# Optimization experiments

Hardware: AMD Instinct MI355X
Metric: run time of the kernel (lower is better)

The kernel has to match this reference:

```python
import jax, jax.numpy as jnp
import numpy as np

B = 4          # graphs
N = 8192       # coarse nodes (2048/graph)
M = 65536      # fine (skip) nodes (16384/graph)
E = 131072     # edges (32768/graph)
T = 16         # global tokens per graph
F_IN = 16      # dim of x and x_skip (concat -> in_channels = 32)
HID, OUT = 32, 16
ED, GD, EMB, H = 3, 1024, 64, 4
K = 3


def _make_pe(t, d):
    # PositionalEncoding buffer (sin/cos), deterministic constant
    position = np.arange(t, dtype=np.float32)[:, None]
    div = np.exp(np.arange(0, d, 2, dtype=np.float32) * (-np.log(10000.0) / d))
    pe = np.zeros((t, d), dtype=np.float32)
    pe[:, 0::2] = np.sin(position * div)
    pe[:, 1::2] = np.cos(position * div)
    return jnp.asarray(pe)


def setup_inputs():
    key = jax.random.key(0)
    ks = jax.random.split(key, 30)
    n, m, e = N // B, M // B, E // B
    inp = {}
    inp['x'] = jax.random.normal(ks[0], (N, F_IN), jnp.float32)
    inp['pos'] = jax.random.normal(ks[1], (N, 3), jnp.float32)
    inp['batch'] = jnp.repeat(jnp.arange(B), n)
    inp['x_skip'] = jax.random.normal(ks[2], (M, F_IN), jnp.float32)
    inp['pos_skip'] = jax.random.normal(ks[3], (M, 3), jnp.float32)
    inp['batch_skip'] = jnp.repeat(jnp.arange(B), m)
    off = jnp.repeat(jnp.arange(B) * m, e)
    inp['edge_index'] = jax.random.randint(ks[4], (2, E), 0, m) + off[None, :]
    inp['global_token'] = jax.random.normal(ks[5], (B * T, GD), jnp.float32)
    def lin(k, o, i, s):
        return jax.random.normal(k, (o, i), jnp.float32) * s
    inp['Wq_w'] = lin(ks[6], EMB, ED, 0.3); inp['Wq_b'] = jnp.zeros((EMB,), jnp.float32)
    inp['Wk_w'] = lin(ks[7], EMB, GD, 0.03); inp['Wk_b'] = jnp.zeros((EMB,), jnp.float32)
    inp['Wv_w'] = lin(ks[8], EMB, GD, 0.03); inp['Wv_b'] = jnp.zeros((EMB,), jnp.float32)
    inp['in_proj_w'] = lin(ks[9], 3 * EMB, EMB, 0.125); inp['in_proj_b'] = jnp.zeros((3 * EMB,), jnp.float32)
    inp['out_w'] = lin(ks[10], EMB, EMB, 0.125); inp['out_b'] = jnp.zeros((EMB,), jnp.float32)
    dims = [(2 * F_IN, HID), (HID, HID), (HID, OUT)]
    for i, (ci, co) in enumerate(dims):
        inp[f'nn_w{i}'] = lin(ks[11 + 3 * i], ci * co, ED + EMB, 0.05)
        inp[f'nn_b{i}'] = jnp.zeros((ci * co,), jnp.float32)
        inp[f'root{i}'] = jax.random.normal(ks[12 + 3 * i], (ci, co), jnp.float32) * (1.0 / np.sqrt(ci))
        inp[f'bias{i}'] = jnp.zeros((co,), jnp.float32)
    return inp


def reference(x, pos, batch, x_skip, pos_skip, batch_skip, edge_index, global_token,
              Wq_w, Wq_b, Wk_w, Wk_b, Wv_w, Wv_b, in_proj_w, in_proj_b, out_w, out_b,
              nn_w0, nn_b0, root0, bias0, nn_w1, nn_b1, root1, bias1, nn_w2, nn_b2, root2, bias2):
    # ---- knn_interpolate (k=3, inverse squared-distance weighting) ----
    # graphs are equal-sized by construction so per-graph knn == batched knn
    pos_b = pos.reshape(B, -1, 3)
    posk_b = pos_skip.reshape(B, -1, 3)
    d2 = ((posk_b ** 2).sum(-1)[:, :, None] + (pos_b ** 2).sum(-1)[:, None, :]
          - 2.0 * jnp.einsum('bmc,bnc->bmn', posk_b, pos_b))  # [B,m,n]
    neg, idx = jax.lax.top_k(-d2, K)                           # [B,m,K]
    w = 1.0 / jnp.maximum(-neg, 1e-16)
    x_b = x.reshape(B, -1, x.shape[-1])
    feats = jnp.take_along_axis(x_b[:, None, :, :], idx[:, :, :, None], axis=2)  # [B,m,K,F]
    xf = ((w[..., None] * feats).sum(2) / w.sum(2)[..., None]).reshape(M, -1)

    src, dst = edge_index[0], edge_index[1]
    pseudo = pos_skip[dst] - pos_skip[src]                     # patch_size is None
    edge_pos = (0.5 * (pos_skip[dst] + pos_skip[src])).reshape(B, -1, 3)
    gt = global_token.reshape(B, -1, global_token.shape[-1])
    pe = _make_pe(gt.shape[1], EMB)
    Q = edge_pos @ Wq_w.T + Wq_b                               # [B,Eb,EMB]
    Kt = gt @ Wk_w.T + Wk_b + pe                               # dropout in eval = identity
    Vt = gt @ Wv_w.T + Wv_b + pe
    # ---- MultiheadAttention (batch_first) ----
    wq, wk, wv = jnp.split(in_proj_w, 3, axis=0)
    bq, bk, bv = jnp.split(in_proj_b, 3, axis=0)
    hd = EMB // H
    def heads(t, w_, b_):
        t = t @ w_.T + b_
        return t.reshape(t.shape[0], t.shape[1], H, hd).transpose(0, 2, 1, 3)
    q, k_, v = heads(Q, wq, bq), heads(Kt, wk, bk), heads(Vt, wv, bv)
    att = jax.nn.softmax(jnp.einsum('bhqd,bhkd->bhqk', q, k_) / np.sqrt(hd).astype(np.float32), axis=-1)
    o = jnp.einsum('bhqk,bhkd->bhqd', att, v).transpose(0, 2, 1, 3).reshape(B, -1, EMB)
    o = o @ out_w.T + out_b
    pseudo = jnp.concatenate([pseudo, o.reshape(-1, EMB)], axis=-1)  # [E, 3+64]

    # ---- NNConv stack (gather -> edge MLP -> per-edge matmul -> scatter mean) ----
    h = jnp.concatenate([xf, x_skip], axis=1)                  # [M, 32]
    ones = jnp.ones((E,), jnp.float32)
    cnt = jnp.maximum(jax.ops.segment_sum(ones, dst, num_segments=M), 1.0)[:, None]
    for nw, nb, rt, bs in ((nn_w0, nn_b0, root0, bias0),
                           (nn_w1, nn_b1, root1, bias1),
                           (nn_w2, nn_b2, root2, bias2)):
        ci, co = rt.shape
        we = jax.nn.relu(pseudo @ nw.T + nb).reshape(E, ci, co)  # MLP (BN at default eval stats ~ identity)
        msg = jnp.einsum('ei,eio->eo', h[src], we)               # [E, co]
        aggr = jax.ops.segment_sum(msg, dst, num_segments=M) / cnt
        h = jax.nn.relu(aggr + h @ rt + bs)                      # drop_act=False -> relu every layer
    return h, pos_skip, batch_skip
```

## Files before the change

### kernel.cpp

```cpp
#include <hip/hip_runtime.h>
#include <math.h>

#define NB    4
#define NN    8192
#define MM    65536
#define EE    131072
#define NPG   2048

typedef short short8 __attribute__((ext_vector_type(8)));
typedef float f32x4  __attribute__((ext_vector_type(4)));

static __device__ inline unsigned short f2b(float f) {
    unsigned u = __float_as_uint(f);
    u += 0x7fffu + ((u >> 16) & 1u);
    return (unsigned short)(u >> 16);
}
static __device__ inline unsigned f2b_pack(float a, float b) {
    unsigned x = __float_as_uint(a); x += 0x7fffu + ((x >> 16) & 1u);
    unsigned y = __float_as_uint(b); y += 0x7fffu + ((y >> 16) & 1u);
    return (x >> 16) | (y & 0xffff0000u);
}
static __device__ inline short8 bc8(uint4 v) {
    union { uint4 u; short8 s; } c; c.u = v; return c.s;
}

__global__ __launch_bounds__(256)
void k_knn(const float* __restrict__ pos, const float* __restrict__ pos_skip,
           const float* __restrict__ x, const float* __restrict__ x_skip,
           const int* __restrict__ batch_skip,
           float* __restrict__ h0, float* __restrict__ out_pos,
           float* __restrict__ out_batch)
{
    __shared__ float4 cp[NPG];
    __shared__ unsigned pk[4][128][3];
    __shared__ float wFin[128][3];
    __shared__ int   iFin[128][3];

    int tid = threadIdx.x;
    int g = blockIdx.x >> 7;
    int cbase = g * NPG;
    for (int c = tid; c < NPG; c += 256) {
        float px = pos[(cbase + c) * 3 + 0];
        float py = pos[(cbase + c) * 3 + 1];
        float pz = pos[(cbase + c) * 3 + 2];
        cp[c] = make_float4(px, py, pz, px * px + py * py + pz * pz);
    }
    __syncthreads();

    int p = tid & 63;
    int slice = tid >> 6;
    int fbase = blockIdx.x * 128;
    int f0 = fbase + p, f1 = fbase + 64 + p;
    float fx0 = pos_skip[f0 * 3 + 0], fy0 = pos_skip[f0 * 3 + 1], fz0 = pos_skip[f0 * 3 + 2];
    float fx1 = pos_skip[f1 * 3 + 0], fy1 = pos_skip[f1 * 3 + 1], fz1 = pos_skip[f1 * 3 + 2];
    float fq0 = fx0 * fx0 + fy0 * fy0 + fz0 * fz0;
    float fq1 = fx1 * fx1 + fy1 * fy1 + fz1 * fz1;

    unsigned ka0 = 0xFFFFFFFFu, ka1 = 0xFFFFFFFFu, ka2 = 0xFFFFFFFFu;
    unsigned kb0 = 0xFFFFFFFFu, kb1 = 0xFFFFFFFFu, kb2 = 0xFFFFFFFFu;
    const float4* cps = cp + slice * 512;
#pragma unroll 8
    for (int l = 0; l < 512; ++l) {
        float4 cc = cps[l];
        float s0 = fx0 * cc.x + fy0 * cc.y + fz0 * cc.z;
        float d0 = fmaxf(fq0 + cc.w - 2.f * s0, 0.f);
        unsigned k = (__float_as_uint(d0) & 0xFFFFFE00u) | (unsigned)l;
        unsigned t1 = max(ka0, k); ka0 = min(ka0, k);
        unsigned t2 = max(ka1, t1); ka1 = min(ka1, t1);
        ka2 = min(ka2, t2);
        float s1 = fx1 * cc.x + fy1 * cc.y + fz1 * cc.z;
        float d1 = fmaxf(fq1 + cc.w - 2.f * s1, 0.f);
        unsigned kq = (__float_as_uint(d1) & 0xFFFFFE00u) | (unsigned)l;
        t1 = max(kb0, kq); kb0 = min(kb0, kq);
        t2 = max(kb1, t1); kb1 = min(kb1, t1);
        kb2 = min(kb2, t2);
    }
    pk[slice][p][0] = ka0; pk[slice][p][1] = ka1; pk[slice][p][2] = ka2;
    pk[slice][64 + p][0] = kb0; pk[slice][64 + p][1] = kb1; pk[slice][64 + p][2] = kb2;
    __syncthreads();

    if (tid < 128) {
        int n = tid;
        int f = fbase + n;
        float gx = pos_skip[f * 3 + 0], gy = pos_skip[f * 3 + 1], gz = pos_skip[f * 3 + 2];
        float gq = gx * gx + gy * gy + gz * gz;
        unsigned long long m0 = ~0ull, m1 = ~0ull, m2 = ~0ull;
#pragma unroll
        for (int s = 0; s < 4; ++s)
#pragma unroll
            for (int r = 0; r < 3; ++r) {
                unsigned key = pk[s][n][r];
                int c = s * 512 + (int)(key & 511u);
                float4 cc = cp[c];
                float d = fmaxf(gq + cc.w - 2.f * (gx * cc.x + gy * cc.y + gz * cc.z), 0.f);
                unsigned long long kk = ((unsigned long long)__float_as_uint(d) << 32) | (unsigned)c;
                unsigned long long t1 = m0 > kk ? m0 : kk; m0 = m0 < kk ? m0 : kk;
                unsigned long long t2 = m1 > t1 ? m1 : t1; m1 = m1 < t1 ? m1 : t1;
                m2 = m2 < t2 ? m2 : t2;
            }
        float d0 = __uint_as_float((unsigned)(m0 >> 32));
        float d1 = __uint_as_float((unsigned)(m1 >> 32));
        float d2 = __uint_as_float((unsigned)(m2 >> 32));
        float w0 = 1.f / fmaxf(d0, 1e-16f);
        float w1 = 1.f / fmaxf(d1, 1e-16f);
        float w2 = 1.f / fmaxf(d2, 1e-16f);
        float inv = 1.f / (w0 + w1 + w2);
        wFin[n][0] = w0 * inv; wFin[n][1] = w1 * inv; wFin[n][2] = w2 * inv;
        iFin[n][0] = cbase + (int)(m0 & 2047u);
        iFin[n][1] = cbase + (int)(m1 & 2047u);
        iFin[n][2] = cbase + (int)(m2 & 2047u);
        out_pos[f * 3 + 0] = gx; out_pos[f * 3 + 1] = gy; out_pos[f * 3 + 2] = gz;
        out_batch[f] = (float)batch_skip[f];
    }
    __syncthreads();

    int n2 = tid >> 1, half = tid & 1;
    int f2 = fbase + n2;
    float4* h04 = (float4*)(h0 + (size_t)f2 * 32);
    if (half == 0) {
        const float4* x4 = (const float4*)x;
        float w0 = wFin[n2][0], w1 = wFin[n2][1], w2 = wFin[n2][2];
        int a0 = iFin[n2][0] * 4, a1 = iFin[n2][1] * 4, a2 = iFin[n2][2] * 4;
#pragma unroll
        for (int j = 0; j < 4; ++j) {
            float4 v0 = x4[a0 + j], v1 = x4[a1 + j], v2 = x4[a2 + j];
            float4 r;
            r.x = w0 * v0.x + w1 * v1.x + w2 * v2.x;
            r.y = w0 * v0.y + w1 * v1.y + w2 * v2.y;
            r.z = w0 * v0.z + w1 * v1.z + w2 * v2.z;
            r.w = w0 * v0.w + w1 * v1.w + w2 * v2.w;
            h04[j] = r;
        }
    } else {
        const float4* xs4 = (const float4*)x_skip;
#pragma unroll
        for (int j = 0; j < 4; ++j) h04[4 + j] = xs4[f2 * 4 + j];
    }
}

__global__ __launch_bounds__(128)
void k_tokens1(const float* __restrict__ gt,
               const float* __restrict__ Wk_w, const float* __restrict__ Wk_b,
               const float* __restrict__ Wv_w, const float* __restrict__ Wv_b,
               float* __restrict__ KtVt)
{
    int b = blockIdx.x >> 4;
    int t = blockIdx.x & 15;
    int which = threadIdx.x >> 6;
    int d = threadIdx.x & 63;
    const float* W = which ? Wv_w : Wk_w;
    const float* bias = which ? Wv_b : Wk_b;
    const float4* row = (const float4*)(gt + (size_t)(b * 16 + t) * 1024);
    const float4* wr = (const float4*)(W + (size_t)d * 1024);
    float acc = 0.f;
    for (int c = 0; c < 256; ++c) {
        float4 a = row[c], w = wr[c];
        acc += a.x * w.x; acc += a.y * w.y; acc += a.z * w.z; acc += a.w * w.w;
    }
    int i2 = d >> 1;
    float dv = expf((float)(2 * i2) * (-0.14391156831212787f));
    float ang = (float)t * dv;
    float pe = (d & 1) ? cosf(ang) : sinf(ang);
    KtVt[((size_t)(b * 2 + which) * 16 + t) * 64 + d] = acc + bias[d] + pe;
}

__global__ __launch_bounds__(256)
void k_tokens2(const float* __restrict__ KtVt,
               const float* __restrict__ in_proj_w, const float* __restrict__ in_proj_b,
               const float* __restrict__ out_w,
               const float* __restrict__ Wq_w, const float* __restrict__ Wq_b,
               float* __restrict__ kall, float* __restrict__ V2,
               float* __restrict__ qW, float* __restrict__ qb2)
{
    int b = blockIdx.x;
    __shared__ float KtL[1024], VtL[1024], vv[1024];
    for (int idx = threadIdx.x; idx < 1024; idx += 256) {
        KtL[idx] = KtVt[(size_t)(b * 2 + 0) * 1024 + idx];
        VtL[idx] = KtVt[(size_t)(b * 2 + 1) * 1024 + idx];
    }
    __syncthreads();
    for (int idx = threadIdx.x; idx < 2048; idx += 256) {
        int which = idx >> 10; int td = idx & 1023; int t = td >> 6; int j = td & 63;
        int r = (which ? 128 : 64) + j;
        const float* w = in_proj_w + (size_t)r * 64;
        const float* src = which ? VtL : KtL;
        float acc = in_proj_b[r];
#pragma unroll 8
        for (int dd = 0; dd < 64; ++dd) acc += src[t * 64 + dd] * w[dd];
        if (which) vv[t * 64 + j] = acc;
        else kall[(size_t)(b * 16 + t) * 64 + j] = acc;
    }
    __syncthreads();
    for (int idx = threadIdx.x; idx < 4096; idx += 256) {
        int jo = idx & 63; int th = idx >> 6; int h = th & 3; int t = th >> 2;
        float acc = 0.f;
#pragma unroll
        for (int dd = 0; dd < 16; ++dd)
            acc += vv[t * 64 + h * 16 + dd] * out_w[(size_t)jo * 64 + h * 16 + dd];
        V2[(((size_t)(b * 16 + t)) * 4 + h) * 64 + jo] = acc;
    }
    if (b == 0) {
        for (int idx = threadIdx.x; idx < 192; idx += 256) {
            int c = idx >> 6; int j = idx & 63;
            float acc = 0.f;
            for (int dd = 0; dd < 64; ++dd) acc += in_proj_w[(size_t)j * 64 + dd] * Wq_w[dd * 3 + c];
            qW[c * 64 + j] = acc;
        }
        for (int j = threadIdx.x; j < 64; j += 256) {
            float acc = in_proj_b[j];
            for (int dd = 0; dd < 64; ++dd) acc += in_proj_w[(size_t)j * 64 + dd] * Wq_b[dd];
            qb2[j] = acc;
        }
    }
}

__global__ __launch_bounds__(256)
void k_edge_attn(const float* __restrict__ ps, const int* __restrict__ ei,
                 const float* __restrict__ kall, const float* __restrict__ V2g,
                 const float* __restrict__ qW, const float* __restrict__ qb2,
                 const float* __restrict__ ob,
                 unsigned short* __restrict__ Pf, float* __restrict__ cnt)
{
    __shared__ __align__(16) float kk[1024];
    __shared__ __align__(16) float v2s[4096];
    __shared__ float qWs[192];
    __shared__ float qbs[64];
    __shared__ __align__(16) float obs[64];
    int g = blockIdx.x >> 7;
    for (int idx = threadIdx.x; idx < 1024; idx += 256) kk[idx] = kall[(size_t)g * 1024 + idx];
    for (int idx = threadIdx.x; idx < 4096; idx += 256) v2s[idx] = V2g[(size_t)g * 4096 + idx];
    if (threadIdx.x < 192) qWs[threadIdx.x] = qW[threadIdx.x];
    if (threadIdx.x < 64) { qbs[threadIdx.x] = qb2[threadIdx.x]; obs[threadIdx.x] = ob[threadIdx.x]; }
    __syncthreads();

    int e = blockIdx.x * 256 + threadIdx.x;
    int s = ei[e], d = ei[EE + e];
    atomicAdd(&cnt[d], 1.f);
    float sx = ps[s * 3], sy = ps[s * 3 + 1], sz = ps[s * 3 + 2];
    float dx = ps[d * 3], dy = ps[d * 3 + 1], dz = ps[d * 3 + 2];
    float px = dx - sx, py = dy - sy, pz = dz - sz;
    float ex = 0.5f * (dx + sx), ey = 0.5f * (dy + sy), ez = 0.5f * (dz + sz);

    float att[4][16];
    const float4* kk4 = (const float4*)kk;
#pragma unroll
    for (int h = 0; h < 4; ++h) {
        float qh[16];
#pragma unroll
        for (int dd = 0; dd < 16; ++dd) {
            int j = h * 16 + dd;
            qh[dd] = qbs[j] + ex * qWs[j] + ey * qWs[64 + j] + ez * qWs[128 + j];
        }
        float sc[16]; float mx = -3.4e38f;
#pragma unroll
        for (int t = 0; t < 16; ++t) {
            float a = 0.f;
#pragma unroll
            for (int qd = 0; qd < 4; ++qd) {
                float4 kv = kk4[t * 16 + h * 4 + qd];
                a += qh[qd * 4 + 0] * kv.x; a += qh[qd * 4 + 1] * kv.y;
                a += qh[qd * 4 + 2] * kv.z; a += qh[qd * 4 + 3] * kv.w;
            }
            a *= 0.25f;
            sc[t] = a; mx = fmaxf(mx, a);
        }
        float ssum = 0.f;
#pragma unroll
        for (int t = 0; t < 16; ++t) { float eo = expf(sc[t] - mx); sc[t] = eo; ssum += eo; }
        float inv = 1.f / ssum;
#pragma unroll
        for (int t = 0; t < 16; ++t) att[h][t] = sc[t] * inv;
    }

    int et = e >> 4, eL = e & 15;
    const float4* v24 = (const float4*)v2s;
#pragma unroll
    for (int q = 0; q < 16; ++q) {
        float4 acc = ((const float4*)obs)[q];
#pragma unroll
        for (int t = 0; t < 16; ++t)
#pragma unroll
            for (int h = 0; h < 4; ++h) {
                float a = att[h][t];
                float4 vq = v24[(t * 4 + h) * 16 + q];
                acc.x += a * vq.x; acc.y += a * vq.y; acc.z += a * vq.z; acc.w += a * vq.w;
            }
        int k0 = q * 4;
        int st = k0 >> 5, quad = (k0 >> 3) & 3, jj = k0 & 7;
        size_t base = ((size_t)(et * 3 + st) * 64 + quad * 16 + eL) * 8 + jj;
        uint2 v; v.x = f2b_pack(acc.x, acc.y); v.y = f2b_pack(acc.z, acc.w);
        *(uint2*)(Pf + base) = v;
    }
    size_t tb = ((size_t)(et * 3 + 2) * 64 + 0 * 16 + eL) * 8;
    uint2 t0; t0.x = f2b_pack(px, py); t0.y = f2b_pack(pz, 1.0f);
    *(uint2*)(Pf + tb) = t0;
    uint2 z2; z2.x = 0u; z2.y = 0u;
    *(uint2*)(Pf + tb + 4) = z2;
#pragma unroll
    for (int quad = 1; quad < 4; ++quad) {
        size_t zb = ((size_t)(et * 3 + 2) * 64 + quad * 16 + eL) * 8;
        uint4 z4; z4.x = 0u; z4.y = 0u; z4.z = 0u; z4.w = 0u;
        *(uint4*)(Pf + zb) = z4;
    }
}

static __device__ inline void repack_one(const float* __restrict__ nw,
                                         const float* __restrict__ nb,
                                         unsigned short* __restrict__ Wf, int idx)
{
    int jj = idx & 7;
    int lane = (idx >> 3) & 63;
    int rest = idx >> 9;
    int s = rest % 3;
    int jt = rest / 3;
    int j = jt * 16 + (lane & 15);
    int k = s * 32 + (lane >> 4) * 8 + jj;
    float v;
    if (k < 64)       v = nw[(size_t)j * 67 + 3 + k];
    else if (k < 67)  v = nw[(size_t)j * 67 + (k - 64)];
    else if (k == 67) v = nb[j];
    else              v = 0.f;
    Wf[idx] = f2b(v);
}

__global__ __launch_bounds__(256)
void k_repackAll(const float* __restrict__ nw0, const float* __restrict__ nb0,
                 const float* __restrict__ nw1, const float* __restrict__ nb1,
                 const float* __restrict__ nw2, const float* __restrict__ nb2,
                 unsigned short* __restrict__ Wf0, unsigned short* __restrict__ Wf1,
                 unsigned short* __restrict__ Wf2)
{
    int idx = blockIdx.x * 256 + threadIdx.x;
    if (idx < 98304)        repack_one(nw0, nb0, Wf0, idx);
    else if (idx < 196608)  repack_one(nw1, nb1, Wf1, idx - 98304);
    else                    repack_one(nw2, nb2, Wf2, idx - 196608);
}

template<int CO>
__global__ __launch_bounds__(256, 4)
void k_conv_mfma(const uint4* __restrict__ Pf, const float* __restrict__ hin,
                 const int* __restrict__ ei, const uint4* __restrict__ Wf,
                 float* __restrict__ aggr)
{
    constexpr int JT = 2 * CO;
    constexpr int NPAR = CO / 16;
    __shared__ float hL[128 * 36];
    __shared__ int sL[128];
    __shared__ int dL[128];

    int tid = threadIdx.x;
    int e0 = blockIdx.x * 128;
    if (tid < 128) sL[tid] = ei[e0 + tid];
    else           dL[tid - 128] = ei[EE + e0 + (tid - 128)];
    __syncthreads();
    for (int idx = tid; idx < 1024; idx += 256) {
        int row = idx >> 3, c = idx & 7;
        const float4* hr = (const float4*)(hin + (size_t)sL[row] * 32);
        *(float4*)&hL[row * 36 + c * 4] = hr[c];
    }
    __syncthreads();

    int wave = tid >> 6, lane = tid & 63, quad = lane >> 4, col = lane & 15;

    uint4 a[2][3];
    int et0 = blockIdx.x * 8 + wave * 2;
#pragma unroll
    for (int st = 0; st < 2; ++st)
#pragma unroll
        for (int s = 0; s < 3; ++s)
            a[st][s] = Pf[((size_t)(et0 + st) * 3 + s) * 64 + lane];

    float msg[2][NPAR][4];
#pragma unroll
    for (int st = 0; st < 2; ++st)
#pragma unroll
        for (int p = 0; p < NPAR; ++p)
#pragma unroll
            for (int r = 0; r < 4; ++r) msg[st][p][r] = 0.f;

#pragma unroll 2
    for (int jt = 0; jt < JT; ++jt) {
        uint4 b0 = Wf[((size_t)jt * 3 + 0) * 64 + lane];
        uint4 b1 = Wf[((size_t)jt * 3 + 1) * 64 + lane];
        uint4 b2 = Wf[((size_t)jt * 3 + 2) * 64 + lane];
        int i   = (CO == 32) ? (jt >> 1) : jt;
        int par = (CO == 32) ? (jt & 1) : 0;
#pragma unroll
        for (int st = 0; st < 2; ++st) {
            f32x4 c = {0.f, 0.f, 0.f, 0.f};
            c = __builtin_amdgcn_mfma_f32_16x16x32_bf16(bc8(a[st][0]), bc8(b0), c, 0, 0, 0);
            c = __builtin_amdgcn_mfma_f32_16x16x32_bf16(bc8(a[st][1]), bc8(b1), c, 0, 0, 0);
            c = __builtin_amdgcn_mfma_f32_16x16x32_bf16(bc8(a[st][2]), bc8(b2), c, 0, 0, 0);
#pragma unroll
            for (int r = 0; r < 4; ++r) {
                float hv = hL[(wave * 32 + st * 16 + quad * 4 + r) * 36 + i];
                msg[st][par][r] += hv * fmaxf(c[r], 0.f);
            }
        }
    }

#pragma unroll
    for (int st = 0; st < 2; ++st)
#pragma unroll
        for (int r = 0; r < 4; ++r) {
            int dv = dL[wave * 32 + st * 16 + quad * 4 + r];
#pragma unroll
            for (int p = 0; p < NPAR; ++p)
                atomicAdd(&aggr[(size_t)dv * CO + p * 16 + col], msg[st][p][r]);
        }
}

template<int CO>
__global__ __launch_bounds__(256)
void k_update(float* __restrict__ aggr, const float* __restrict__ cnt,
              const float* __restrict__ hin, const float* __restrict__ root,
              const float* __restrict__ bias, float* __restrict__ hout)
{
    __shared__ float rL[32 * CO];
    __shared__ float bL[CO];
    int tid = threadIdx.x;
    for (int idx = tid; idx < 32 * CO; idx += 256) rL[idx] = root[idx];
    if (tid < CO) bL[tid] = bias[tid];
    __syncthreads();
    int gid = blockIdx.x * 256 + tid;
    int v = gid / CO;
    int o = gid % CO;
    float acc = aggr[gid] / fmaxf(cnt[v], 1.f) + bL[o];
    aggr[gid] = 0.f;
    const float* hr = hin + (size_t)v * 32;
#pragma unroll
    for (int i = 0; i < 32; ++i) acc += hr[i] * rL[i * CO + o];
    hout[gid] = fmaxf(acc, 0.f);
}

extern "C" void kernel_launch(void* const* d_in, const int* in_sizes, int n_in,
                              void* d_out, int out_size, void* d_ws, size_t ws_size,
                              hipStream_t stream)
{
    const float* x          = (const float*)d_in[0];
    const float* pos        = (const float*)d_in[1];
    const float* x_skip     = (const float*)d_in[3];
    const float* pos_skip   = (const float*)d_in[4];
    const int*   batch_skip = (const int*)  d_in[5];
    const int*   ei         = (const int*)  d_in[6];
    const float* gt         = (const float*)d_in[7];
    const float* Wq_w       = (const float*)d_in[8];
    const float* Wq_b       = (const float*)d_in[9];
    const float* Wk_w       = (const float*)d_in[10];
    const float* Wk_b       = (const float*)d_in[11];
    const float* Wv_w       = (const float*)d_in[12];
    const float* Wv_b       = (const float*)d_in[13];
    const float* in_proj_w  = (const float*)d_in[14];
    const float* in_proj_b  = (const float*)d_in[15];
    const float* out_w      = (const float*)d_in[16];
    const float* out_b      = (const float*)d_in[17];
    const float* nn_w0 = (const float*)d_in[18]; const float* nn_b0 = (const float*)d_in[19];
    const float* root0 = (const float*)d_in[20]; const float* bias0 = (const float*)d_in[21];
    const float* nn_w1 = (const float*)d_in[22]; const float* nn_b1 = (const float*)d_in[23];
    const float* root1 = (const float*)d_in[24]; const float* bias1 = (const float*)d_in[25];
    const float* nn_w2 = (const float*)d_in[26]; const float* nn_b2 = (const float*)d_in[27];
    const float* root2 = (const float*)d_in[28]; const float* bias2 = (const float*)d_in[29];

    char* wsb = (char*)d_ws;
    size_t off = 0;
    auto carve = [&](size_t bytes) { char* p = wsb + off; off += (bytes + 255) & ~(size_t)255; return p; };
    float* aggr = (float*)carve((size_t)MM * 32 * 4);
    float* cnt  = (float*)carve((size_t)MM * 4);
    float* hA   = (float*)carve((size_t)MM * 32 * 4);
    float* hB   = (float*)carve((size_t)MM * 32 * 4);
    unsigned short* Pf  = (unsigned short*)carve((size_t)EE * 96 * 2);
    unsigned short* Wf0 = (unsigned short*)carve((size_t)1024 * 96 * 2);
    unsigned short* Wf1 = (unsigned short*)carve((size_t)1024 * 96 * 2);
    unsigned short* Wf2 = (unsigned short*)carve((size_t)512 * 96 * 2);
    float* kall = (float*)carve((size_t)NB * 16 * 64 * 4);
    float* V2   = (float*)carve((size_t)NB * 16 * 4 * 64 * 4);
    float* qW   = (float*)carve(192 * 4);
    float* qb2  = (float*)carve(64 * 4);
    float* KtVt = (float*)carve((size_t)NB * 2 * 16 * 64 * 4);

    float* h_final   = (float*)d_out;
    float* out_pos   = (float*)d_out + (size_t)MM * 16;
    float* out_batch = (float*)d_out + (size_t)MM * 19;

    hipMemsetAsync(aggr, 0, ((size_t)MM * 32 + MM) * sizeof(float), stream);

    k_tokens1<<<64, 128, 0, stream>>>(gt, Wk_w, Wk_b, Wv_w, Wv_b, KtVt);
    k_tokens2<<<NB, 256, 0, stream>>>(KtVt, in_proj_w, in_proj_b, out_w, Wq_w, Wq_b,
                                      kall, V2, qW, qb2);
    k_knn<<<MM / 128, 256, 0, stream>>>(pos, pos_skip, x, x_skip, batch_skip,
                                        hA, out_pos, out_batch);
    k_edge_attn<<<EE / 256, 256, 0, stream>>>(pos_skip, ei, kall, V2, qW, qb2, out_b,
                                              Pf, cnt);
    k_repackAll<<<960, 256, 0, stream>>>(nn_w0, nn_b0, nn_w1, nn_b1, nn_w2, nn_b2,
                                         Wf0, Wf1, Wf2);

    k_conv_mfma<32><<<EE / 128, 256, 0, stream>>>((const uint4*)Pf, hA, ei, (const uint4*)Wf0, aggr);
    k_update<32><<<(MM * 32) / 256, 256, 0, stream>>>(aggr, cnt, hA, root0, bias0, hB);
    k_conv_mfma<32><<<EE / 128, 256, 0, stream>>>((const uint4*)Pf, hB, ei, (const uint4*)Wf1, aggr);
    k_update<32><<<(MM * 32) / 256, 256, 0, stream>>>(aggr, cnt, hB, root1, bias1, hA);
    k_conv_mfma<16><<<EE / 128, 256, 0, stream>>>((const uint4*)Pf, hA, ei, (const uint4*)Wf2, aggr);
    k_update<16><<<(MM * 16) / 256, 256, 0, stream>>>(aggr, cnt, hA, root2, bias2, h_final);
}
```

Measured before the change: 425.7 us.

## Fold query projection into keys and compute edge attention output with MFMA

Attention scores are now linear in the edge midpoint. The query weights are folded into the projected keys per graph in k_tokens2, giving a 64x4 matrix Mfold, so each edge computes its 64 scores with 4 FMAs each instead of forming q and doing dot products. The attention-times-V2 product moves from per-thread scalar FMAs to bf16 MFMA 16x16x32, with attention weights staged through LDS and V2 prepacked in bf16 fragment layout. This removes most per-edge ALU work and LDS loads, at the cost of bf16 rounding of the attention weights and extra LDS round trips for the transposed output stores.

After: 388.8 us. 1.09x faster.

```diff
diff --git a/kernel.cpp b/kernel.cpp
--- a/kernel.cpp
+++ b/kernel.cpp
@@ -169,17 +169,19 @@
                const float* __restrict__ in_proj_w, const float* __restrict__ in_proj_b,
                const float* __restrict__ out_w,
                const float* __restrict__ Wq_w, const float* __restrict__ Wq_b,
-               float* __restrict__ kall, float* __restrict__ V2,
-               float* __restrict__ qW, float* __restrict__ qb2)
+               float* __restrict__ Mfold, uint4* __restrict__ v2fG)
 {
     int b = blockIdx.x;
-    __shared__ float KtL[1024], VtL[1024], vv[1024];
-    for (int idx = threadIdx.x; idx < 1024; idx += 256) {
+    int tid = threadIdx.x;
+    __shared__ float KtL[1024], VtL[1024], vv[1024], kproj[1024];
+    __shared__ float v2L[4096];
+    __shared__ float qWs[192], qbs[64];
+    for (int idx = tid; idx < 1024; idx += 256) {
         KtL[idx] = KtVt[(size_t)(b * 2 + 0) * 1024 + idx];
         VtL[idx] = KtVt[(size_t)(b * 2 + 1) * 1024 + idx];
     }
     __syncthreads();
-    for (int idx = threadIdx.x; idx < 2048; idx += 256) {
+    for (int idx = tid; idx < 2048; idx += 256) {
         int which = idx >> 10; int td = idx & 1023; int t = td >> 6; int j = td & 63;
         int r = (which ? 128 : 64) + j;
         const float* w = in_proj_w + (size_t)r * 64;
@@ -188,52 +190,66 @@
 #pragma unroll 8
         for (int dd = 0; dd < 64; ++dd) acc += src[t * 64 + dd] * w[dd];
         if (which) vv[t * 64 + j] = acc;
-        else kall[(size_t)(b * 16 + t) * 64 + j] = acc;
-    }
-    __syncthreads();
-    for (int idx = threadIdx.x; idx < 4096; idx += 256) {
-        int jo = idx & 63; int th = idx >> 6; int h = th & 3; int t = th >> 2;
+        else kproj[t * 64 + j] = acc;
+    }
+    for (int idx = tid; idx < 192; idx += 256) {
+        int c = idx >> 6; int j = idx & 63;
+        float acc = 0.f;
+        for (int dd = 0; dd < 64; ++dd) acc += in_proj_w[(size_t)j * 64 + dd] * Wq_w[dd * 3 + c];
+        qWs[c * 64 + j] = acc;
+    }
+    for (int j = tid; j < 64; j += 256) {
+        float acc = in_proj_b[j];
+        for (int dd = 0; dd < 64; ++dd) acc += in_proj_w[(size_t)j * 64 + dd] * Wq_b[dd];
+        qbs[j] = acc;
+    }
+    __syncthreads();
+    for (int idx = tid; idx < 4096; idx += 256) {
+        int jo = idx & 63; int th2 = idx >> 6; int h = th2 & 3; int t = th2 >> 2;
         float acc = 0.f;
 #pragma unroll
         for (int dd = 0; dd < 16; ++dd)
             acc += vv[t * 64 + h * 16 + dd] * out_w[(size_t)jo * 64 + h * 16 + dd];
-        V2[(((size_t)(b * 16 + t)) * 4 + h) * 64 + jo] = acc;
-    }
-    if (b == 0) {
-        for (int idx = threadIdx.x; idx < 192; idx += 256) {
-            int c = idx >> 6; int j = idx & 63;
-            float acc = 0.f;
-            for (int dd = 0; dd < 64; ++dd) acc += in_proj_w[(size_t)j * 64 + dd] * Wq_w[dd * 3 + c];
-            qW[c * 64 + j] = acc;
-        }
-        for (int j = threadIdx.x; j < 64; j += 256) {
-            float acc = in_proj_b[j];
-            for (int dd = 0; dd < 64; ++dd) acc += in_proj_w[(size_t)j * 64 + dd] * Wq_b[dd];
-            qb2[j] = acc;
-        }
+        v2L[(t * 4 + h) * 64 + jo] = acc;
+    }
+    {
+        int th = tid >> 2, c = tid & 3;
+        int t = th >> 2, h = th & 3;
+        float acc = 0.f;
+#pragma unroll
+        for (int dd = h * 16; dd < h * 16 + 16; ++dd) {
+            float w = (c == 0) ? qWs[dd] : (c == 1) ? qWs[64 + dd]
+                    : (c == 2) ? qWs[128 + dd] : qbs[dd];
+            acc += w * kproj[t * 64 + dd];
+        }
+        Mfold[((size_t)b * 64 + th) * 4 + c] = 0.25f * acc;
+    }
+    __syncthreads();
+    for (int it = tid; it < 512; it += 256) {
+        int lane = it & 63, fi = it >> 6;
+        int mi = fi >> 1, step = fi & 1;
+        int outd = mi * 16 + (lane & 15);
+        int th0 = step * 32 + (lane >> 4) * 8;
+        uint4 v;
+        v.x = f2b_pack(v2L[(th0 + 0) * 64 + outd], v2L[(th0 + 1) * 64 + outd]);
+        v.y = f2b_pack(v2L[(th0 + 2) * 64 + outd], v2L[(th0 + 3) * 64 + outd]);
+        v.z = f2b_pack(v2L[(th0 + 4) * 64 + outd], v2L[(th0 + 5) * 64 + outd]);
+        v.w = f2b_pack(v2L[(th0 + 6) * 64 + outd], v2L[(th0 + 7) * 64 + outd]);
+        v2fG[((size_t)b * 8 + fi) * 64 + lane] = v;
     }
 }
 
 __global__ __launch_bounds__(256)
 void k_edge_attn(const float* __restrict__ ps, const int* __restrict__ ei,
-                 const float* __restrict__ kall, const float* __restrict__ V2g,
-                 const float* __restrict__ qW, const float* __restrict__ qb2,
+                 const float* __restrict__ Mfold, const uint4* __restrict__ v2f,
                  const float* __restrict__ ob,
                  unsigned short* __restrict__ Pf, float* __restrict__ cnt)
 {
-    __shared__ __align__(16) float kk[1024];
-    __shared__ __align__(16) float v2s[4096];
-    __shared__ float qWs[192];
-    __shared__ float qbs[64];
-    __shared__ __align__(16) float obs[64];
+    __shared__ unsigned attL[4 * 64 * 34];
+    int tid = threadIdx.x;
+    int wave = tid >> 6, lane = tid & 63, q = lane >> 4, c15 = lane & 15;
     int g = blockIdx.x >> 7;
-    for (int idx = threadIdx.x; idx < 1024; idx += 256) kk[idx] = kall[(size_t)g * 1024 + idx];
-    for (int idx = threadIdx.x; idx < 4096; idx += 256) v2s[idx] = V2g[(size_t)g * 4096 + idx];
-    if (threadIdx.x < 192) qWs[threadIdx.x] = qW[threadIdx.x];
-    if (threadIdx.x < 64) { qbs[threadIdx.x] = qb2[threadIdx.x]; obs[threadIdx.x] = ob[threadIdx.x]; }
-    __syncthreads();
-
-    int e = blockIdx.x * 256 + threadIdx.x;
+    int e = blockIdx.x * 256 + tid;
     int s = ei[e], d = ei[EE + e];
     atomicAdd(&cnt[d], 1.f);
     float sx = ps[s * 3], sy = ps[s * 3 + 1], sz = ps[s * 3 + 2];
@@ -241,64 +257,98 @@
     float px = dx - sx, py = dy - sy, pz = dz - sz;
     float ex = 0.5f * (dx + sx), ey = 0.5f * (dy + sy), ez = 0.5f * (dz + sz);
 
-    float att[4][16];
-    const float4* kk4 = (const float4*)kk;
+    const float4* Mg = (const float4*)Mfold + (size_t)g * 64;
+    float sc[64];
+#pragma unroll
+    for (int th = 0; th < 64; ++th) {
+        float4 m = Mg[th];
+        sc[th] = ex * m.x + ey * m.y + ez * m.z + m.w;
+    }
 #pragma unroll
     for (int h = 0; h < 4; ++h) {
-        float qh[16];
-#pragma unroll
-        for (int dd = 0; dd < 16; ++dd) {
-            int j = h * 16 + dd;
-            qh[dd] = qbs[j] + ex * qWs[j] + ey * qWs[64 + j] + ez * qWs[128 + j];
-        }
-        float sc[16]; float mx = -3.4e38f;
+        float mx = sc[h];
+#pragma unroll
+        for (int t = 1; t < 16; ++t) mx = fmaxf(mx, sc[t * 4 + h]);
+        float ssum = 0.f;
 #pragma unroll
         for (int t = 0; t < 16; ++t) {
-            float a = 0.f;
-#pragma unroll
-            for (int qd = 0; qd < 4; ++qd) {
-                float4 kv = kk4[t * 16 + h * 4 + qd];
-                a += qh[qd * 4 + 0] * kv.x; a += qh[qd * 4 + 1] * kv.y;
-                a += qh[qd * 4 + 2] * kv.z; a += qh[qd * 4 + 3] * kv.w;
-            }
-            a *= 0.25f;
-            sc[t] = a; mx = fmaxf(mx, a);
-        }
-        float ssum = 0.f;
-#pragma unroll
-        for (int t = 0; t < 16; ++t) { float eo = expf(sc[t] - mx); sc[t] = eo; ssum += eo; }
+            float eo = expf(sc[t * 4 + h] - mx);
+            sc[t * 4 + h] = eo; ssum += eo;
+        }
         float inv = 1.f / ssum;
 #pragma unroll
-        for (int t = 0; t < 16; ++t) att[h][t] = sc[t] * inv;
-    }
-
-    int et = e >> 4, eL = e & 15;
-    const float4* v24 = (const float4*)v2s;
-#pragma unroll
-    for (int q = 0; q < 16; ++q) {
-        float4 acc = ((const float4*)obs)[q];
-#pragma unroll
-        for (int t = 0; t < 16; ++t)
-#pragma unroll
-            for (int h = 0; h < 4; ++h) {
-                float a = att[h][t];
-                float4 vq = v24[(t * 4 + h) * 16 + q];
-                acc.x += a * vq.x; acc.y += a * vq.y; acc.z += a * vq.z; acc.w += a * vq.w;
-            }
-        int k0 = q * 4;
-        int st = k0 >> 5, quad = (k0 >> 3) & 3, jj = k0 & 7;
-        size_t base = ((size_t)(et * 3 + st) * 64 + quad * 16 + eL) * 8 + jj;
-        uint2 v; v.x = f2b_pack(acc.x, acc.y); v.y = f2b_pack(acc.z, acc.w);
-        *(uint2*)(Pf + base) = v;
-    }
-    size_t tb = ((size_t)(et * 3 + 2) * 64 + 0 * 16 + eL) * 8;
+        for (int t = 0; t < 16; ++t) sc[t * 4 + h] *= inv;
+    }
+    unsigned* slab = attL + wave * 64 * 34;
+#pragma unroll
+    for (int k = 0; k < 16; ++k) {
+        uint2 v;
+        v.x = f2b_pack(sc[4 * k + 0], sc[4 * k + 1]);
+        v.y = f2b_pack(sc[4 * k + 2], sc[4 * k + 3]);
+        *(uint2*)&slab[lane * 34 + 2 * k] = v;
+    }
+    __syncthreads();
+
+    uint4 v2a[4][2];
+#pragma unroll
+    for (int mi = 0; mi < 4; ++mi)
+#pragma unroll
+        for (int st = 0; st < 2; ++st)
+            v2a[mi][st] = v2f[((size_t)g * 8 + mi * 2 + st) * 64 + lane];
+
+    f32x4 acc[4][4];
+#pragma unroll
+    for (int mi = 0; mi < 4; ++mi)
+#pragma unroll
+        for (int nt = 0; nt < 4; ++nt) acc[mi][nt] = (f32x4){0.f, 0.f, 0.f, 0.f};
+
+#pragma unroll
+    for (int nt = 0; nt < 4; ++nt) {
+        const unsigned* rb = &slab[(nt * 16 + c15) * 34];
+        uint4 b0 = *(const uint4*)&rb[q * 4];
+        uint4 b1 = *(const uint4*)&rb[16 + q * 4];
+#pragma unroll
+        for (int mi = 0; mi < 4; ++mi) {
+            acc[mi][nt] = __builtin_amdgcn_mfma_f32_16x16x32_bf16(bc8(v2a[mi][0]), bc8(b0), acc[mi][nt], 0, 0, 0);
+            acc[mi][nt] = __builtin_amdgcn_mfma_f32_16x16x32_bf16(bc8(v2a[mi][1]), bc8(b1), acc[mi][nt], 0, 0, 0);
+        }
+    }
+    __syncthreads();
+
+    float4 obv[4];
+#pragma unroll
+    for (int mi = 0; mi < 4; ++mi) obv[mi] = *(const float4*)(ob + mi * 16 + q * 4);
+#pragma unroll
+    for (int mi = 0; mi < 4; ++mi)
+#pragma unroll
+        for (int nt = 0; nt < 4; ++nt) {
+            f32x4 a = acc[mi][nt];
+            uint2 v;
+            v.x = f2b_pack(a[0] + obv[mi].x, a[1] + obv[mi].y);
+            v.y = f2b_pack(a[2] + obv[mi].z, a[3] + obv[mi].w);
+            *(uint2*)&slab[(nt * 16 + c15) * 34 + mi * 8 + q * 2] = v;
+        }
+    __syncthreads();
+
+    uint4* Pf4 = (uint4*)Pf;
+#pragma unroll
+    for (int et = 0; et < 4; ++et) {
+        int etg = blockIdx.x * 16 + wave * 4 + et;
+#pragma unroll
+        for (int st = 0; st < 2; ++st) {
+            uint4 w = *(const uint4*)&slab[(et * 16 + c15) * 34 + st * 16 + q * 4];
+            Pf4[((size_t)etg * 3 + st) * 64 + lane] = w;
+        }
+    }
+    int et2 = e >> 4, eL = e & 15;
+    size_t tb = ((size_t)(et2 * 3 + 2) * 64 + 0 * 16 + eL) * 8;
     uint2 t0; t0.x = f2b_pack(px, py); t0.y = f2b_pack(pz, 1.0f);
     *(uint2*)(Pf + tb) = t0;
     uint2 z2; z2.x = 0u; z2.y = 0u;
     *(uint2*)(Pf + tb + 4) = z2;
 #pragma unroll
     for (int quad = 1; quad < 4; ++quad) {
-        size_t zb = ((size_t)(et * 3 + 2) * 64 + quad * 16 + eL) * 8;
+        size_t zb = ((size_t)(et2 * 3 + 2) * 64 + quad * 16 + eL) * 8;
         uint4 z4; z4.x = 0u; z4.y = 0u; z4.z = 0u; z4.w = 0u;
         *(uint4*)(Pf + zb) = z4;
     }
@@ -472,11 +522,9 @@
     unsigned short* Wf0 = (unsigned short*)carve((size_t)1024 * 96 * 2);
     unsigned short* Wf1 = (unsigned short*)carve((size_t)1024 * 96 * 2);
     unsigned short* Wf2 = (unsigned short*)carve((size_t)512 * 96 * 2);
-    float* kall = (float*)carve((size_t)NB * 16 * 64 * 4);
-    float* V2   = (float*)carve((size_t)NB * 16 * 4 * 64 * 4);
-    float* qW   = (float*)carve(192 * 4);
-    float* qb2  = (float*)carve(64 * 4);
-    float* KtVt = (float*)carve((size_t)NB * 2 * 16 * 64 * 4);
+    float* Mfold = (float*)carve((size_t)NB * 64 * 4 * 4);
+    uint4* v2f   = (uint4*)carve((size_t)NB * 8 * 64 * 16);
+    float* KtVt  = (float*)carve((size_t)NB * 2 * 16 * 64 * 4);
 
     float* h_final   = (float*)d_out;
     float* out_pos   = (float*)d_out + (size_t)MM * 16;
@@ -486,10 +534,10 @@
 
     k_tokens1<<<64, 128, 0, stream>>>(gt, Wk_w, Wk_b, Wv_w, Wv_b, KtVt);
     k_tokens2<<<NB, 256, 0, stream>>>(KtVt, in_proj_w, in_proj_b, out_w, Wq_w, Wq_b,
-                                      kall, V2, qW, qb2);
+                                      Mfold, v2f);
     k_knn<<<MM / 128, 256, 0, stream>>>(pos, pos_skip, x, x_skip, batch_skip,
                                         hA, out_pos, out_batch);
-    k_edge_attn<<<EE / 256, 256, 0, stream>>>(pos_skip, ei, kall, V2, qW, qb2, out_b,
+    k_edge_attn<<<EE / 256, 256, 0, stream>>>(pos_skip, ei, Mfold, v2f, out_b,
                                               Pf, cnt);
     k_repackAll<<<960, 256, 0, stream>>>(nn_w0, nn_b0, nn_w1, nn_b1, nn_w2, nn_b2,
                                          Wf0, Wf1, Wf2);
```
